# Kernel tuning notes

Hardware: AMD Instinct MI355X
Metric: run time of the kernel (lower is better)

The kernel has to match this reference:

```python
import jax, jax.numpy as jnp
import numpy as np

S, B, I, O, H, E, K = 128, 32, 512, 512, 512, 8, 2


def setup_inputs() -> dict:
    key = jax.random.key(0)
    ks = jax.random.split(key, 6)
    s = 0.02
    return {
        "x": jax.random.normal(ks[0], (S, B, I), dtype=jnp.float32),
        "router_w": jax.random.normal(ks[1], (I, E), dtype=jnp.float32) * s,
        "router_b": jnp.zeros((E,), dtype=jnp.float32),
        # per-expert LSTM controller params (proxy for DNC_Adapted recurrent expert)
        "Wi": jax.random.normal(ks[2], (E, I, 4 * H), dtype=jnp.float32) * s,
        "Wh": jax.random.normal(ks[3], (E, H, 4 * H), dtype=jnp.float32) * s,
        "b": jnp.zeros((E, 4 * H), dtype=jnp.float32),
        "Wo": jax.random.normal(ks[4], (E, H, O), dtype=jnp.float32) * s,
        "bo": jnp.zeros((E, O), dtype=jnp.float32),
    }


def _expert(x_seq, Wi, Wh, b, Wo, bo):
    # x_seq: [S, B, I] (dense, zero-padded at non-routed positions, as in the
    # original per-expert dispatch); single-layer LSTM controller + output proj.
    Bsz = x_seq.shape[1]
    Hd = Wh.shape[0]

    def step(carry, xt):
        h, c = carry
        gates = xt @ Wi + h @ Wh + b            # [B, 4H]
        i_, f_, g_, o_ = jnp.split(gates, 4, axis=-1)
        c = jax.nn.sigmoid(f_) * c + jax.nn.sigmoid(i_) * jnp.tanh(g_)
        h = jax.nn.sigmoid(o_) * jnp.tanh(c)
        return (h, c), h @ Wo + bo              # [B, O]

    init = (jnp.zeros((Bsz, Hd), x_seq.dtype), jnp.zeros((Bsz, Hd), x_seq.dtype))
    _, ys = jax.lax.scan(step, init, x_seq)
    return ys                                   # [S, B, O]


def reference(x, router_w, router_b, Wi, Wh, b, Wo, bo):
    S_, B_, I_ = x.shape
    N = S_ * B_
    flat_x = x.reshape(N, I_)
    logits = flat_x @ router_w + router_b        # [N, E]
    top_vals, top_idx = jax.lax.top_k(logits, K) # [N, K]
    rw = jax.nn.softmax(top_vals, axis=1)        # routing weights over top-k

    # mask[k, e, n] = 1 if token n routed to expert e at rank k
    mask = (top_idx.T[:, None, :] == jnp.arange(E)[None, :, None]).astype(x.dtype)
    # dense zero-padded per-(k, expert) inputs, matching the original dispatch
    expert_x = (mask[..., None] * flat_x[None, None]).reshape(K, E, S_, B_, I_)

    run_e = jax.vmap(_expert, in_axes=(0, 0, 0, 0, 0, 0))            # over experts
    run_ke = jax.vmap(run_e, in_axes=(0, None, None, None, None, None))  # over k
    out = run_ke(expert_x, Wi, Wh, b, Wo, bo)    # [K, E, S, B, O]
    out = out.reshape(K, E, N, -1)

    # scatter-add weighted expert outputs back to token positions
    y = jnp.einsum('ken,nk,keno->no', mask, rw, out)
    return y.reshape(S_, B_, -1)
```

## Files before the change

kernel.cpp:

```cpp
#include <hip/hip_runtime.h>
#include <hip/hip_bf16.h>
#include <cstdint>
#include <cstddef>

#define DI __device__ __forceinline__

typedef __bf16 bf16_t;
typedef bf16_t bf16x8 __attribute__((ext_vector_type(8)));
typedef float f32x4 __attribute__((ext_vector_type(4)));
typedef unsigned int u32;
typedef unsigned long long u64;

constexpr int S_ = 128, B_ = 32, I_ = 512, H_ = 512, O_ = 512, E_ = 8;
constexpr int Ntok = S_ * B_;
constexpr int G4 = 4 * H_;
constexpr int ROWS = 64;
constexpr int SLOT = E_ * ROWS * H_;

constexpr size_t OFF_CNT  = 0;
constexpr size_t OFF_XCDM = 64;
constexpr size_t OFF_XCDG = 704;
constexpr size_t OFF_DFL  = 1024;
constexpr size_t OFF_MASK = 2048;
constexpr size_t OFF_FLG  = 10240;
constexpr size_t OFF_HALL = 16384;
constexpr size_t SLOT_B   = (size_t)SLOT * 2;
constexpr size_t ZERO_BYTES = OFF_HALL + SLOT_B;
constexpr size_t OFF_TIDX = OFF_HALL + 129ull * SLOT_B;
constexpr size_t OFF_RW   = OFF_TIDX + (size_t)Ntok * 2 * 4;
constexpr size_t OFF_LIST = OFF_RW + (size_t)Ntok * 2 * 4;
constexpr size_t OFF_WHT  = OFF_LIST + (size_t)E_ * Ntok * 4;
constexpr size_t OFF_WIT  = OFF_WHT + (size_t)E_ * G4 * H_ * 2;
constexpr size_t OFF_WOT  = OFF_WIT + (size_t)E_ * G4 * I_ * 2;
constexpr size_t OFF_XP   = OFF_WOT + (size_t)E_ * O_ * H_ * 2;
constexpr size_t WS_NEED  = OFF_XP + (size_t)Ntok * 2 * G4 * 2;

DI float sigf(float v) { return 1.f / (1.f + __expf(-v)); }
DI float tanh_(float v) { float e = __expf(2.f * v); return 1.f - 2.f / (e + 1.f); }
DI float bfu(u32 s) { u32 x = (s & 0xffffu) << 16; return __builtin_bit_cast(float, x); }

DI bf16x8 pack8(float4 a, float4 b) {
  bf16x8 r;
  r[0] = (bf16_t)a.x; r[1] = (bf16_t)a.y; r[2] = (bf16_t)a.z; r[3] = (bf16_t)a.w;
  r[4] = (bf16_t)b.x; r[5] = (bf16_t)b.y; r[6] = (bf16_t)b.z; r[7] = (bf16_t)b.w;
  return r;
}

__global__ void k_prep(const float* __restrict__ src, bf16_t* __restrict__ dst,
                       int Cdim, int perm) {
  __shared__ float tile[32][33];
  int ct = blockIdx.x, kt = blockIdx.y, e = blockIdx.z;
  const float* se = src + (size_t)e * 512 * Cdim;
  bf16_t* de = dst + (size_t)e * Cdim * 512;
  int c = threadIdx.x & 31, r0 = threadIdx.x >> 5;
  for (int s = 0; s < 4; s++) {
    int rr = r0 + s * 8;
    tile[rr][c] = se[(size_t)(kt * 32 + rr) * Cdim + ct * 32 + c];
  }
  __syncthreads();
  int kk = threadIdx.x & 31, c0 = threadIdx.x >> 5;
  for (int s = 0; s < 4; s++) {
    int cc = c0 + s * 8;
    int cg = ct * 32 + cc;
    int vc = perm ? (((cg & 511) >> 4) * 64 + (cg >> 9) * 16 + (cg & 15)) : cg;
    int kg = kt * 32 + kk;
    de[(size_t)vc * 512 + (kg ^ ((vc & 7) << 3))] = (bf16_t)tile[kk][cc];
  }
}

__global__ void k_router(const float* __restrict__ x, const float* __restrict__ rww,
                         const float* __restrict__ rwb, int* __restrict__ topidx,
                         float* __restrict__ rwgt, int* __restrict__ lists,
                         int* __restrict__ cnt, u64* __restrict__ rowmask) {
  int n = blockIdx.x * 4 + (threadIdx.x >> 6);
  int l = threadIdx.x & 63;
  const float* xr = x + (size_t)n * I_;
  double acc[8] = {0, 0, 0, 0, 0, 0, 0, 0};
  for (int ii = 0; ii < 8; ii++) {
    int i = l * 8 + ii;
    double xv = (double)xr[i];
    const float* wr = rww + i * 8;
#pragma unroll
    for (int e = 0; e < 8; e++) acc[e] += xv * (double)wr[e];
  }
#pragma unroll
  for (int off = 32; off > 0; off >>= 1)
#pragma unroll
    for (int e = 0; e < 8; e++) acc[e] += __shfl_xor(acc[e], off, 64);
  if (l == 0) {
    double lg[8];
    for (int e = 0; e < 8; e++) lg[e] = acc[e] + (double)rwb[e];
    int e0 = 0;
    for (int e = 1; e < 8; e++) if (lg[e] > lg[e0]) e0 = e;
    int e1 = -1;
    for (int e = 0; e < 8; e++) { if (e == e0) continue; if (e1 < 0 || lg[e] > lg[e1]) e1 = e; }
    double ed = exp(lg[e1] - lg[e0]);
    float p0 = (float)(1.0 / (1.0 + ed));
    float p1 = (float)(ed / (1.0 + ed));
    topidx[n * 2] = e0; topidx[n * 2 + 1] = e1;
    rwgt[n * 2] = p0; rwgt[n * 2 + 1] = p1;
    int t = n >> 5, bi = n & 31;
    int p = atomicAdd(&cnt[e0], 1); lists[e0 * Ntok + p] = n * 2;
    p = atomicAdd(&cnt[e1], 1);     lists[e1 * Ntok + p] = n * 2 + 1;
    atomicOr(&rowmask[e0 * 128 + t], 1ull << bi);
    atomicOr(&rowmask[e1 * 128 + t], 1ull << (32 + bi));
  }
}

DI void gemm64(const bf16_t* Als, const bf16_t* Bls, int wv, int l, f32x4* acc) {
  int ar = l & 15, kg = l >> 4;
  int arow = wv * 16 + ar;
  int aswz = (ar & 7) << 3;
#pragma unroll
  for (int ks = 0; ks < 16; ks++) {
    int kb = ks * 32 + kg * 8;
    bf16x8 a = *(const bf16x8*)&Als[arow * 512 + (kb ^ aswz)];
#pragma unroll
    for (int q = 0; q < 4; q++) {
      bf16x8 b = *(const bf16x8*)&Bls[(q * 16 + ar) * 512 + (kb ^ aswz)];
      acc[q] = __builtin_amdgcn_mfma_f32_16x16x32_bf16(a, b, acc[q], 0, 0, 0);
    }
  }
}

__launch_bounds__(256, 1)
__global__ void k_xp(const float* __restrict__ x, const bf16_t* __restrict__ Wit,
                     const int* __restrict__ lists, const int* __restrict__ cnt,
                     bf16_t* __restrict__ xp2) {
  __shared__ bf16_t Als[64 * 512];
  __shared__ bf16_t Bls[64 * 512];
  __shared__ int ents[64];
  int e = blockIdx.z, ct = blockIdx.x, rt0 = blockIdx.y;
  int count = cnt[e];
  int tid = threadIdx.x;
  const bf16_t* bs = Wit + ((size_t)e * G4 + ct * 64) * 512;
#pragma unroll
  for (int i2 = 0; i2 < 16; i2++) {
    int o = (i2 * 256 + tid) * 8;
    *(bf16x8*)&Bls[o] = *(const bf16x8*)&bs[o];
  }
  int l = tid & 63, wv = tid >> 6;
  int rr = tid >> 2, qq = tid & 3;
  int swzr = (rr & 7) << 3;
  for (int rbase = rt0 * 64; rbase < count; rbase += 16 * 64) {
    __syncthreads();
    if (tid < 64) ents[tid] = (rbase + tid < count) ? lists[e * Ntok + rbase + tid] : -1;
    __syncthreads();
    int ent = ents[rr];
    if (ent >= 0) {
      const float* xr = x + (size_t)(ent >> 1) * I_ + qq * 128;
#pragma unroll
      for (int i2 = 0; i2 < 16; i2++) {
        float4 a = *(const float4*)(xr + i2 * 8);
        float4 b = *(const float4*)(xr + i2 * 8 + 4);
        *(bf16x8*)&Als[rr * 512 + ((qq * 128 + i2 * 8) ^ swzr)] = pack8(a, b);
      }
    } else {
      bf16x8 z;
      for (int jz = 0; jz < 8; jz++) z[jz] = (bf16_t)0.f;
#pragma unroll
      for (int i2 = 0; i2 < 16; i2++)
        *(bf16x8*)&Als[rr * 512 + ((qq * 128 + i2 * 8) ^ swzr)] = z;
    }
    __syncthreads();
    f32x4 acc[4];
    for (int q = 0; q < 4; q++) { f32x4 z = {0.f, 0.f, 0.f, 0.f}; acc[q] = z; }
    gemm64(Als, Bls, wv, l, acc);
#pragma unroll
    for (int q = 0; q < 4; q++)
#pragma unroll
      for (int r = 0; r < 4; r++) {
        int rr2 = wv * 16 + ((l >> 4) << 2) + r;
        int ent2 = ents[rr2];
        if (ent2 >= 0) {
          int g = ct * 64 + q * 16 + (l & 15);
          xp2[(size_t)ent2 * G4 + (size_t)(g & 511) * 4 + (g >> 9)] = (bf16_t)acc[q][r];
        }
      }
  }
}

__launch_bounds__(256, 1)
__global__ void k_rec(const bf16_t* __restrict__ Wht, const bf16_t* __restrict__ xp2,
                      const float* __restrict__ bgate, bf16_t* __restrict__ hall,
                      const u64* __restrict__ rowmask, u32* __restrict__ flags,
                      u32* __restrict__ dfl, u32* __restrict__ xcdm,
                      u32* __restrict__ xcdg) {
  __shared__ bf16_t Bls[64 * 512];
  int bid = blockIdx.x;
  int e = bid & 7, w = bid >> 3;
  int tid = threadIdx.x, l = tid & 63, wv = tid >> 6;
  const bf16_t* bs = Wht + ((size_t)e * G4 + w * 64) * 512;
#pragma unroll
  for (int i2 = 0; i2 < 16; i2++) {
    int o = (i2 * 256 + tid) * 8;
    *(bf16x8*)&Bls[o] = *(const bf16x8*)&bs[o];
  }
  int jl = l & 15, j = w * 16 + jl;
  float bq[4];
#pragma unroll
  for (int q = 0; q < 4; q++) bq[q] = bgate[e * G4 + q * 512 + j];
  int xcd = __builtin_amdgcn_s_getreg(20 | (3 << 11)) & 15;
  if (tid == 0) {
    __hip_atomic_fetch_or(&xcdm[e * 16], 1u << xcd, __ATOMIC_RELAXED, __HIP_MEMORY_SCOPE_AGENT);
    __hip_atomic_fetch_or(xcdg, 1u << xcd, __ATOMIC_RELAXED, __HIP_MEMORY_SCOPE_AGENT);
    __hip_atomic_store(&dfl[e * 32 + w], 1u, __ATOMIC_RELEASE, __HIP_MEMORY_SCOPE_AGENT);
  }
  for (;;) {
    u32 f = __hip_atomic_load(&dfl[e * 32 + (l & 31)], __ATOMIC_RELAXED, __HIP_MEMORY_SCOPE_AGENT);
    if (__all((int)(f >= 1u))) break;
    __builtin_amdgcn_s_sleep(1);
  }
  __builtin_amdgcn_sched_barrier(0);
  u32 me = __hip_atomic_load(&xcdm[e * 16], __ATOMIC_RELAXED, __HIP_MEMORY_SCOPE_AGENT);
  u32 mg = __hip_atomic_load(xcdg, __ATOMIC_RELAXED, __HIP_MEMORY_SCOPE_AGENT);
  bool fast = (__popc(me) == 1) && (__popc(mg) > 1);
  __syncthreads();

  float creg[4] = {0.f, 0.f, 0.f, 0.f};
  int ar = l & 15, kg = l >> 4;
  int arow = wv * 16 + ar;
  int aswz = (ar & 7) << 3;
  int r0 = wv * 16 + (kg << 2);
  const ushort* xpu = (const ushort*)xp2;

  uint2 xpc[4], xpn[4];
  {
    u64 mk = rowmask[e * 128];
#pragma unroll
    for (int r = 0; r < 4; r++) {
      int row = r0 + r;
      xpc[r].x = 0; xpc[r].y = 0;
      if ((mk >> row) & 1ull) {
        int n2 = ((row & 31)) * 2 + (row >> 5);
        xpc[r] = *(const uint2*)(xpu + ((size_t)n2 * G4 + j * 4));
      }
    }
  }

  for (int t = 0; t < 128; t++) {
    const bf16_t* hc = hall + (size_t)t * SLOT + e * ROWS * 512;
    bf16x8 af[16];
#pragma unroll
    for (int ks = 0; ks < 16; ks++)
      af[ks] = *(const bf16x8*)&hc[arow * 512 + ks * 32 + kg * 8];
#pragma unroll
    for (int r = 0; r < 4; r++) { xpn[r].x = 0; xpn[r].y = 0; }
    if (t < 127) {
      u64 mk = rowmask[e * 128 + t + 1];
#pragma unroll
      for (int r = 0; r < 4; r++) {
        int row = r0 + r;
        if ((mk >> row) & 1ull) {
          int n2 = (((t + 1) << 5) + (row & 31)) * 2 + (row >> 5);
          xpn[r] = *(const uint2*)(xpu + ((size_t)n2 * G4 + j * 4));
        }
      }
    }
    f32x4 acc[4];
    for (int q = 0; q < 4; q++) { f32x4 z = {0.f, 0.f, 0.f, 0.f}; acc[q] = z; }
#pragma unroll
    for (int ks = 0; ks < 16; ks++) {
      int kb = ks * 32 + kg * 8;
#pragma unroll
      for (int q = 0; q < 4; q++) {
        bf16x8 b = *(const bf16x8*)&Bls[(q * 16 + ar) * 512 + (kb ^ aswz)];
        acc[q] = __builtin_amdgcn_mfma_f32_16x16x32_bf16(af[ks], b, acc[q], 0, 0, 0);
      }
    }
    bf16_t* hn = hall + (size_t)(t + 1) * SLOT + e * ROWS * 512;
#pragma unroll
    for (int r = 0; r < 4; r++) {
      int row = r0 + r;
      float gi = acc[0][r] + bq[0] + bfu(xpc[r].x);
      float gf = acc[1][r] + bq[1] + bfu(xpc[r].x >> 16);
      float gg = acc[2][r] + bq[2] + bfu(xpc[r].y);
      float go = acc[3][r] + bq[3] + bfu(xpc[r].y >> 16);
      float cn = sigf(gf) * creg[r] + sigf(gi) * tanh_(gg);
      creg[r] = cn;
      hn[row * 512 + j] = (bf16_t)(sigf(go) * tanh_(cn));
    }
#pragma unroll
    for (int r = 0; r < 4; r++) xpc[r] = xpn[r];
    if (t < 127) {
      __syncthreads();
      if (!fast) __threadfence();
      if (tid == 0)
        __hip_atomic_store(&flags[e * 64 + w], (u32)(t + 1), __ATOMIC_RELAXED,
                           __HIP_MEMORY_SCOPE_AGENT);
      u32 tgt = (u32)(t + 1);
      for (;;) {
        u32 f = __hip_atomic_load(&flags[e * 64 + (l & 31)], __ATOMIC_RELAXED,
                                  __HIP_MEMORY_SCOPE_AGENT);
        if (__all((int)(f >= tgt))) break;
        __builtin_amdgcn_s_sleep(1);
      }
      __builtin_amdgcn_sched_barrier(0);
      if (!fast) __threadfence();
    }
  }
}

__launch_bounds__(256, 1)
__global__ void k_out(const bf16_t* __restrict__ hall, const bf16_t* __restrict__ Wot,
                      const float* __restrict__ bo, const int* __restrict__ lists,
                      const int* __restrict__ cnt, const float* __restrict__ rwgt,
                      float* __restrict__ y) {
  __shared__ bf16_t Als[64 * 512];
  __shared__ bf16_t Bls[64 * 512];
  __shared__ int ents[64];
  __shared__ float rws[64];
  int e = blockIdx.z, ct = blockIdx.x, rt0 = blockIdx.y;
  int count = cnt[e];
  int tid = threadIdx.x;
  const bf16_t* bsrc = Wot + ((size_t)e * O_ + ct * 64) * 512;
#pragma unroll
  for (int i2 = 0; i2 < 16; i2++) {
    int o = (i2 * 256 + tid) * 8;
    *(bf16x8*)&Bls[o] = *(const bf16x8*)&bsrc[o];
  }
  int l = tid & 63, wv = tid >> 6;
  int rr = tid >> 2, qq = tid & 3;
  int swzr = (rr & 7) << 3;
  float boq[4];
#pragma unroll
  for (int q = 0; q < 4; q++) boq[q] = bo[e * O_ + ct * 64 + q * 16 + (l & 15)];
  for (int rbase = rt0 * 64; rbase < count; rbase += 16 * 64) {
    __syncthreads();
    if (tid < 64) {
      int ent = (rbase + tid < count) ? lists[e * Ntok + rbase + tid] : -1;
      ents[tid] = ent;
      rws[tid] = (ent >= 0) ? rwgt[ent] : 0.f;
    }
    __syncthreads();
    int ent = ents[rr];
    if (ent >= 0) {
      int n = ent >> 1, kk = ent & 1, t = n >> 5;
      const bf16_t* hr = hall + (size_t)(t + 1) * SLOT +
                         (size_t)(e * ROWS + kk * 32 + (n & 31)) * 512 + qq * 128;
#pragma unroll
      for (int i2 = 0; i2 < 16; i2++) {
        bf16x8 v = *(const bf16x8*)(hr + i2 * 8);
        *(bf16x8*)&Als[rr * 512 + ((qq * 128 + i2 * 8) ^ swzr)] = v;
      }
    } else {
      bf16x8 z;
      for (int jz = 0; jz < 8; jz++) z[jz] = (bf16_t)0.f;
#pragma unroll
      for (int i2 = 0; i2 < 16; i2++)
        *(bf16x8*)&Als[rr * 512 + ((qq * 128 + i2 * 8) ^ swzr)] = z;
    }
    __syncthreads();
    f32x4 acc[4];
    for (int q = 0; q < 4; q++) { f32x4 z = {0.f, 0.f, 0.f, 0.f}; acc[q] = z; }
    gemm64(Als, Bls, wv, l, acc);
#pragma unroll
    for (int q = 0; q < 4; q++)
#pragma unroll
      for (int r = 0; r < 4; r++) {
        int rr2 = wv * 16 + ((l >> 4) << 2) + r;
        int ent2 = ents[rr2];
        if (ent2 >= 0) {
          float val = (acc[q][r] + boq[q]) * rws[rr2];
          unsafeAtomicAdd(&y[(size_t)(ent2 >> 1) * O_ + ct * 64 + q * 16 + (l & 15)], val);
        }
      }
  }
}

extern "C" void kernel_launch(void* const* d_in, const int* in_sizes, int n_in,
                              void* d_out, int out_size, void* d_ws, size_t ws_size,
                              hipStream_t stream) {
  (void)in_sizes; (void)n_in;
  const float* x   = (const float*)d_in[0];
  const float* rww = (const float*)d_in[1];
  const float* rwb = (const float*)d_in[2];
  const float* Wi  = (const float*)d_in[3];
  const float* Wh  = (const float*)d_in[4];
  const float* bg  = (const float*)d_in[5];
  const float* Wo  = (const float*)d_in[6];
  const float* bo  = (const float*)d_in[7];
  float* y = (float*)d_out;
  char* ws = (char*)d_ws;

  if (ws_size < WS_NEED) {
    hipMemsetAsync(d_out, 0, (size_t)out_size * 4, stream);
    return;
  }

  int* cnt     = (int*)(ws + OFF_CNT);
  u32* xcdm    = (u32*)(ws + OFF_XCDM);
  u32* xcdg    = (u32*)(ws + OFF_XCDG);
  u32* dfl     = (u32*)(ws + OFF_DFL);
  u64* rowmask = (u64*)(ws + OFF_MASK);
  u32* flags   = (u32*)(ws + OFF_FLG);
  bf16_t* hall = (bf16_t*)(ws + OFF_HALL);
  int* topidx  = (int*)(ws + OFF_TIDX);
  float* rwgt  = (float*)(ws + OFF_RW);
  int* lists   = (int*)(ws + OFF_LIST);
  bf16_t* Wht  = (bf16_t*)(ws + OFF_WHT);
  bf16_t* Wit  = (bf16_t*)(ws + OFF_WIT);
  bf16_t* Wot  = (bf16_t*)(ws + OFF_WOT);
  bf16_t* xp2  = (bf16_t*)(ws + OFF_XP);

  hipMemsetAsync(ws, 0, ZERO_BYTES, stream);
  hipMemsetAsync(d_out, 0, (size_t)out_size * 4, stream);

  k_prep<<<dim3(G4 / 32, 16, 8), 256, 0, stream>>>(Wi, Wit, G4, 0);
  k_prep<<<dim3(G4 / 32, 16, 8), 256, 0, stream>>>(Wh, Wht, G4, 1);
  k_prep<<<dim3(O_ / 32, 16, 8), 256, 0, stream>>>(Wo, Wot, O_, 0);
  k_router<<<Ntok / 4, 256, 0, stream>>>(x, rww, rwb, topidx, rwgt, lists, cnt, rowmask);
  k_xp<<<dim3(32, 16, 8), 256, 0, stream>>>(x, Wit, lists, cnt, xp2);
  k_rec<<<256, 256, 0, stream>>>(Wht, xp2, bg, hall, rowmask, flags, dfl, xcdm, xcdg);
  k_out<<<dim3(8, 16, 8), 256, 0, stream>>>(hall, Wot, bo, lists, cnt, rwgt, y);
}
```

Before: 987.2 us.

## Hold recurrent weights in registers and use per-wave fine-grained step flags

The recurrent kernel now runs 512 threads per block. Each wave keeps its slice of the Wh weights resident in registers instead of LDS. Pairs of waves split the four gates and exchange the activated gates through a small LDS buffer using workgroup-scope flags. The block-wide barrier plus all-to-all flag wait after each timestep is replaced by per-wave flags: a wave publishes its own flag and, at the start of the next step, waits only for the flags of the waves producing the rows it reads. This is meant to cut per-step synchronisation latency and LDS traffic, at the cost of heavy register pressure, spin-waits inside the workgroup, and a more delicate memory-ordering protocol.

```diff
diff --git a/kernel.cpp b/kernel.cpp
--- a/kernel.cpp
+++ b/kernel.cpp
@@ -23,7 +23,7 @@
 constexpr size_t OFF_DFL  = 1024;
 constexpr size_t OFF_MASK = 2048;
 constexpr size_t OFF_FLG  = 10240;
-constexpr size_t OFF_HALL = 16384;
+constexpr size_t OFF_HALL = 32768;
 constexpr size_t SLOT_B   = (size_t)SLOT * 2;
 constexpr size_t ZERO_BYTES = OFF_HALL + SLOT_B;
 constexpr size_t OFF_TIDX = OFF_HALL + 129ull * SLOT_B;
@@ -47,7 +47,7 @@
 }
 
 __global__ void k_prep(const float* __restrict__ src, bf16_t* __restrict__ dst,
-                       int Cdim, int perm) {
+                       int Cdim, int perm, int swz) {
   __shared__ float tile[32][33];
   int ct = blockIdx.x, kt = blockIdx.y, e = blockIdx.z;
   const float* se = src + (size_t)e * 512 * Cdim;
@@ -64,7 +64,8 @@
     int cg = ct * 32 + cc;
     int vc = perm ? (((cg & 511) >> 4) * 64 + (cg >> 9) * 16 + (cg & 15)) : cg;
     int kg = kt * 32 + kk;
-    de[(size_t)vc * 512 + (kg ^ ((vc & 7) << 3))] = (bf16_t)tile[kk][cc];
+    int kg2 = swz ? (kg ^ ((vc & 7) << 3)) : kg;
+    de[(size_t)vc * 512 + kg2] = (bf16_t)tile[kk][cc];
   }
 }
 
@@ -180,26 +181,36 @@
   }
 }
 
-__launch_bounds__(256, 1)
+__launch_bounds__(512, 2)
 __global__ void k_rec(const bf16_t* __restrict__ Wht, const bf16_t* __restrict__ xp2,
                       const float* __restrict__ bgate, bf16_t* __restrict__ hall,
                       const u64* __restrict__ rowmask, u32* __restrict__ flags,
                       u32* __restrict__ dfl, u32* __restrict__ xcdm,
                       u32* __restrict__ xcdg) {
-  __shared__ bf16_t Bls[64 * 512];
+  __shared__ float Gx[4][5632];
+  __shared__ u32 gfl[8];
   int bid = blockIdx.x;
   int e = bid & 7, w = bid >> 3;
   int tid = threadIdx.x, l = tid & 63, wv = tid >> 6;
-  const bf16_t* bs = Wht + ((size_t)e * G4 + w * 64) * 512;
-#pragma unroll
-  for (int i2 = 0; i2 < 16; i2++) {
-    int o = (i2 * 256 + tid) * 8;
-    *(bf16x8*)&Bls[o] = *(const bf16x8*)&bs[o];
-  }
-  int jl = l & 15, j = w * 16 + jl;
-  float bq[4];
-#pragma unroll
-  for (int q = 0; q < 4; q++) bq[q] = bgate[e * G4 + q * 512 + j];
+  int ri = wv >> 1, qi = wv & 1;
+  int jl = l & 15, lg = l >> 4;
+
+  if (tid < 8) gfl[tid] = 0;
+
+  bf16x8 b[2][16];
+  {
+    const bf16_t* bp = Wht + ((size_t)e * G4 + w * 64 + (2 * qi) * 16 + jl) * 512 + lg * 8;
+#pragma unroll
+    for (int qt = 0; qt < 2; qt++)
+#pragma unroll
+      for (int ks = 0; ks < 16; ks++)
+        b[qt][ks] = *(const bf16x8*)(bp + (size_t)qt * 16 * 512 + ks * 32);
+  }
+  float bqv[2];
+#pragma unroll
+  for (int qt = 0; qt < 2; qt++)
+    bqv[qt] = bgate[e * G4 + (2 * qi + qt) * 512 + w * 16 + jl];
+
   int xcd = __builtin_amdgcn_s_getreg(20 | (3 << 11)) & 15;
   if (tid == 0) {
     __hip_atomic_fetch_or(&xcdm[e * 16], 1u << xcd, __ATOMIC_RELAXED, __HIP_MEMORY_SCOPE_AGENT);
@@ -217,86 +228,102 @@
   bool fast = (__popc(me) == 1) && (__popc(mg) > 1);
   __syncthreads();
 
-  float creg[4] = {0.f, 0.f, 0.f, 0.f};
-  int ar = l & 15, kg = l >> 4;
-  int arow = wv * 16 + ar;
-  int aswz = (ar & 7) << 3;
-  int r0 = wv * 16 + (kg << 2);
   const ushort* xpu = (const ushort*)xp2;
-
+  int fidx = e * 256 + (l >> 1) * 8 + ri * 2 + (l & 1);
+  int myflag = e * 256 + w * 8 + ri * 2 + qi;
+  float creg[2] = {0.f, 0.f};
+  float nl0[4], nl1[4];
   uint2 xpc[4], xpn[4];
+
   {
     u64 mk = rowmask[e * 128];
 #pragma unroll
     for (int r = 0; r < 4; r++) {
-      int row = r0 + r;
+      int row = 16 * ri + lg * 4 + r;
       xpc[r].x = 0; xpc[r].y = 0;
       if ((mk >> row) & 1ull) {
-        int n2 = ((row & 31)) * 2 + (row >> 5);
-        xpc[r] = *(const uint2*)(xpu + ((size_t)n2 * G4 + j * 4));
+        int n2 = (row & 31) * 2 + (row >> 5);
+        xpc[r] = *(const uint2*)(xpu + (size_t)n2 * G4 + (size_t)(w * 16 + jl) * 4);
       }
     }
   }
 
   for (int t = 0; t < 128; t++) {
-    const bf16_t* hc = hall + (size_t)t * SLOT + e * ROWS * 512;
-    bf16x8 af[16];
-#pragma unroll
-    for (int ks = 0; ks < 16; ks++)
-      af[ks] = *(const bf16x8*)&hc[arow * 512 + ks * 32 + kg * 8];
 #pragma unroll
     for (int r = 0; r < 4; r++) { xpn[r].x = 0; xpn[r].y = 0; }
     if (t < 127) {
       u64 mk = rowmask[e * 128 + t + 1];
 #pragma unroll
       for (int r = 0; r < 4; r++) {
-        int row = r0 + r;
+        int row = 16 * ri + lg * 4 + r;
         if ((mk >> row) & 1ull) {
           int n2 = (((t + 1) << 5) + (row & 31)) * 2 + (row >> 5);
-          xpn[r] = *(const uint2*)(xpu + ((size_t)n2 * G4 + j * 4));
+          xpn[r] = *(const uint2*)(xpu + (size_t)n2 * G4 + (size_t)(w * 16 + jl) * 4);
         }
       }
     }
-    f32x4 acc[4];
-    for (int q = 0; q < 4; q++) { f32x4 z = {0.f, 0.f, 0.f, 0.f}; acc[q] = z; }
+    for (;;) {
+      u32 f = __hip_atomic_load(&flags[fidx], __ATOMIC_RELAXED, __HIP_MEMORY_SCOPE_AGENT);
+      if (__all((int)(f >= (u32)t))) break;
+      __builtin_amdgcn_s_sleep(1);
+    }
+    __builtin_amdgcn_sched_barrier(0);
+
+    const bf16_t* hb = hall + (size_t)t * SLOT +
+                       (size_t)(e * ROWS + 16 * ri + jl) * 512 + lg * 8;
+    bf16x8 af[4];
+#pragma unroll
+    for (int p = 0; p < 4; p++) af[p] = *(const bf16x8*)(hb + p * 32);
+    f32x4 acc[2];
+    { f32x4 z = {0.f, 0.f, 0.f, 0.f}; acc[0] = z; acc[1] = z; }
 #pragma unroll
     for (int ks = 0; ks < 16; ks++) {
-      int kb = ks * 32 + kg * 8;
-#pragma unroll
-      for (int q = 0; q < 4; q++) {
-        bf16x8 b = *(const bf16x8*)&Bls[(q * 16 + ar) * 512 + (kb ^ aswz)];
-        acc[q] = __builtin_amdgcn_mfma_f32_16x16x32_bf16(af[ks], b, acc[q], 0, 0, 0);
-      }
-    }
+      bf16x8 a = af[ks & 3];
+      if (ks + 4 < 16) af[ks & 3] = *(const bf16x8*)(hb + (ks + 4) * 32);
+      acc[0] = __builtin_amdgcn_mfma_f32_16x16x32_bf16(a, b[0][ks], acc[0], 0, 0, 0);
+      acc[1] = __builtin_amdgcn_mfma_f32_16x16x32_bf16(a, b[1][ks], acc[1], 0, 0, 0);
+    }
+
+#pragma unroll
+    for (int r = 0; r < 4; r++) {
+      u32 xw = qi ? xpc[r].y : xpc[r].x;
+      float g0 = acc[0][r] + bqv[0] + bfu(xw);
+      float g1 = acc[1][r] + bqv[1] + bfu(xw >> 16);
+      nl0[r] = qi ? tanh_(g0) : sigf(g0);
+      nl1[r] = sigf(g1);
+    }
+#pragma unroll
+    for (int r = 0; r < 4; r++) {
+      float2 v = {nl0[r], nl1[r]};
+      *(float2*)&Gx[ri][(lg * 4 + r) * 68 + jl * 4 + qi * 2] = v;
+    }
+    __hip_atomic_store(&gfl[ri * 2 + qi], (u32)(t + 1), __ATOMIC_RELEASE, __HIP_MEMORY_SCOPE_WORKGROUP);
+    while (__hip_atomic_load(&gfl[ri * 2 + (1 - qi)], __ATOMIC_ACQUIRE, __HIP_MEMORY_SCOPE_WORKGROUP) < (u32)(t + 1)) {}
+    __builtin_amdgcn_sched_barrier(0);
+
     bf16_t* hn = hall + (size_t)(t + 1) * SLOT + e * ROWS * 512;
 #pragma unroll
-    for (int r = 0; r < 4; r++) {
-      int row = r0 + r;
-      float gi = acc[0][r] + bq[0] + bfu(xpc[r].x);
-      float gf = acc[1][r] + bq[1] + bfu(xpc[r].x >> 16);
-      float gg = acc[2][r] + bq[2] + bfu(xpc[r].y);
-      float go = acc[3][r] + bq[3] + bfu(xpc[r].y >> 16);
-      float cn = sigf(gf) * creg[r] + sigf(gi) * tanh_(gg);
-      creg[r] = cn;
-      hn[row * 512 + j] = (bf16_t)(sigf(go) * tanh_(cn));
+    for (int rr2 = 0; rr2 < 2; rr2++) {
+      int r = qi * 2 + rr2;
+      float2 oth = *(const float2*)&Gx[ri][(lg * 4 + r) * 68 + jl * 4 + (1 - qi) * 2];
+      float I = qi ? oth.x : nl0[r];
+      float F = qi ? oth.y : nl1[r];
+      float G = qi ? nl0[r] : oth.x;
+      float O = qi ? nl1[r] : oth.y;
+      float cn = F * creg[rr2] + I * G;
+      creg[rr2] = cn;
+      int row = 16 * ri + lg * 4 + r;
+      hn[(size_t)row * 512 + w * 16 + jl] = (bf16_t)(O * tanh_(cn));
     }
 #pragma unroll
     for (int r = 0; r < 4; r++) xpc[r] = xpn[r];
+
     if (t < 127) {
-      __syncthreads();
+      asm volatile("s_waitcnt vmcnt(0)" ::: "memory");
       if (!fast) __threadfence();
-      if (tid == 0)
-        __hip_atomic_store(&flags[e * 64 + w], (u32)(t + 1), __ATOMIC_RELAXED,
+      if (l == 0)
+        __hip_atomic_store(&flags[myflag], (u32)(t + 1), __ATOMIC_RELAXED,
                            __HIP_MEMORY_SCOPE_AGENT);
-      u32 tgt = (u32)(t + 1);
-      for (;;) {
-        u32 f = __hip_atomic_load(&flags[e * 64 + (l & 31)], __ATOMIC_RELAXED,
-                                  __HIP_MEMORY_SCOPE_AGENT);
-        if (__all((int)(f >= tgt))) break;
-        __builtin_amdgcn_s_sleep(1);
-      }
-      __builtin_amdgcn_sched_barrier(0);
-      if (!fast) __threadfence();
     }
   }
 }
@@ -406,11 +433,11 @@
   hipMemsetAsync(ws, 0, ZERO_BYTES, stream);
   hipMemsetAsync(d_out, 0, (size_t)out_size * 4, stream);
 
-  k_prep<<<dim3(G4 / 32, 16, 8), 256, 0, stream>>>(Wi, Wit, G4, 0);
-  k_prep<<<dim3(G4 / 32, 16, 8), 256, 0, stream>>>(Wh, Wht, G4, 1);
-  k_prep<<<dim3(O_ / 32, 16, 8), 256, 0, stream>>>(Wo, Wot, O_, 0);
+  k_prep<<<dim3(G4 / 32, 16, 8), 256, 0, stream>>>(Wi, Wit, G4, 0, 1);
+  k_prep<<<dim3(G4 / 32, 16, 8), 256, 0, stream>>>(Wh, Wht, G4, 1, 0);
+  k_prep<<<dim3(O_ / 32, 16, 8), 256, 0, stream>>>(Wo, Wot, O_, 0, 1);
   k_router<<<Ntok / 4, 256, 0, stream>>>(x, rww, rwb, topidx, rwgt, lists, cnt, rowmask);
   k_xp<<<dim3(32, 16, 8), 256, 0, stream>>>(x, Wit, lists, cnt, xp2);
-  k_rec<<<256, 256, 0, stream>>>(Wht, xp2, bg, hall, rowmask, flags, dfl, xcdm, xcdg);
+  k_rec<<<256, 512, 0, stream>>>(Wht, xp2, bg, hall, rowmask, flags, dfl, xcdm, xcdg);
   k_out<<<dim3(8, 16, 8), 256, 0, stream>>>(hall, Wot, bo, lists, cnt, rwgt, y);
 }
```

After: 2.133 ms. 116% more time.
